# Kernel optimization log

Hardware: AMD Instinct MI355X
Metric: run time of the kernel (lower is better)

Reference implementation:

```python
import jax, jax.numpy as jnp
import numpy as np

DIM = 768
HEADS = 12
HD = DIM // HEADS
E = 8
R = 64
ALPHA = 128.0
LORA_SCALE = ALPHA / R  # 2.0
ENABLE_BITS = np.array([1.0, 0.0, 1.0], dtype=np.float32)  # LoRA on q and v slices of qkv


def setup_inputs() -> dict:
    key = jax.random.key(0)
    ks = jax.random.split(key, 8)
    x = jax.random.normal(ks[0], (2, 4096, DIM), jnp.float32)
    # base (frozen) weights, shared across experts; no biases (qkv_bias=False)
    Wqkv = jax.random.normal(ks[1], (3 * DIM, DIM), jnp.float32) * 0.02
    Wproj = jax.random.normal(ks[2], (DIM, DIM), jnp.float32) * 0.02
    # per-expert LoRA adapters. qkv: shared down-proj A, per-output-slice up-proj B,
    # masked by enable bits (q,k,v).
    Aqkv = jax.random.normal(ks[3], (E, R, DIM), jnp.float32) * 0.02
    Bqkv = jax.random.normal(ks[4], (E, 3, DIM, R), jnp.float32) * 0.02
    Bqkv = Bqkv * jnp.asarray(ENABLE_BITS)[None, :, None, None]
    Aproj = jax.random.normal(ks[5], (E, R, DIM), jnp.float32) * 0.02
    Bproj = jax.random.normal(ks[6], (E, DIM, R), jnp.float32) * 0.02
    expert_indices = np.arange(4, dtype=np.int64) % E  # static per-chunk routing
    chunk_sizes = np.array([1024, 1024, 1024, 1024], dtype=np.int64)
    return {"x": x, "Wqkv": Wqkv, "Aqkv": Aqkv, "Bqkv": Bqkv, "Wproj": Wproj,
            "Aproj": Aproj, "Bproj": Bproj, "expert_indices": expert_indices,
            "chunk_sizes": chunk_sizes}


def reference(x, Wqkv, Aqkv, Bqkv, Wproj, Aproj, Bproj, expert_indices, chunk_sizes):
    # chunk sizes / expert indices are static host-side routing metadata
    sizes = [int(c) for c in np.asarray(chunk_sizes)]
    eidx = [int(e) for e in np.asarray(expert_indices)]
    offs = np.concatenate([[0], np.cumsum(sizes)])
    B = x.shape[0]
    scale = HD ** -0.5
    last_k = None
    last_v = None
    outs = []
    for i, n in enumerate(sizes):
        xc = x[:, offs[i]:offs[i + 1]]            # [B, n, DIM]
        e = eidx[i]
        # LoRA-adapted qkv for this chunk's expert
        base = xc @ Wqkv.T                        # [B, n, 3*DIM]
        h = xc @ Aqkv[e].T                        # [B, n, R]
        delta = jnp.einsum('bnr,tdr->bntd', h, Bqkv[e]).reshape(B, n, 3 * DIM)
        qkv = (base + LORA_SCALE * delta).reshape(B, n, 3, HEADS, HD)
        qkv = qkv.transpose(2, 0, 3, 1, 4)        # [3, B, H, n, HD]
        q, k, v = qkv[0], qkv[1], qkv[2]
        if last_k is not None:                    # growing KV over chunks (chunk-causal)
            k = jnp.concatenate([last_k, k], axis=-2)
            v = jnp.concatenate([last_v, v], axis=-2)
        last_k, last_v = k, v
        attn = jax.nn.softmax(jnp.einsum('bhqd,bhkd->bhqk', q * scale, k), axis=-1)
        o = jnp.einsum('bhqk,bhkd->bhqd', attn, v)
        o = o.transpose(0, 2, 1, 3).reshape(B, n, DIM)
        # LoRA-adapted output projection for the same expert
        o = o @ Wproj.T + LORA_SCALE * ((o @ Aproj[e].T) @ Bproj[e].T)
        outs.append(o)
    return jnp.concatenate(outs, axis=1)          # [B, total, DIM]
```

## Files before the change

### kernel.cpp

```cpp
#include <hip/hip_runtime.h>
#include <hip/hip_bf16.h>
#include <math.h>

#define BATCH   2
#define SEQ     4096
#define DIMD    768
#define NHEADS  12
#define HDIM    64
#define RR      64
#define CHUNK   1024
#define NTOK    (BATCH * SEQ)
#define BHN     (BATCH * NHEADS)
#define KC2     2304
#define QSCALE  0.18033688011112042f

typedef __attribute__((ext_vector_type(8))) short short8;
typedef __attribute__((ext_vector_type(4))) float f32x4;

#define AS1 __attribute__((address_space(1)))
#define AS3 __attribute__((address_space(3)))

__device__ __forceinline__ void glds16(const void* g, void* l) {
    __builtin_amdgcn_global_load_lds((const AS1 unsigned int*)g,
                                     (AS3 unsigned int*)l, 16, 0, 0);
}

__device__ __forceinline__ unsigned pk2u(float a, float b) {
    float2 t; t.x = a; t.y = b;
    __hip_bfloat162 r = __float22bfloat162_rn(t);
    union { __hip_bfloat162 b2; unsigned u; } c; c.b2 = r;
    return c.u;
}
__device__ __forceinline__ float lo16f(unsigned p) { return __uint_as_float(p << 16); }
__device__ __forceinline__ float hi16f(unsigned p) { return __uint_as_float(p & 0xffff0000u); }

__global__ __launch_bounds__(256)
void combine_split(const float* __restrict__ W, const float* __restrict__ A,
                   const float* __restrict__ Bm, int NB,
                   unsigned short* __restrict__ out)
{
    const int tid = threadIdx.x;
    const int ty = tid >> 4, tx = tid & 15;
    const int f0 = blockIdx.x * 64, d0 = blockIdx.y * 64, e = blockIdx.z;

    __shared__ float Bb[64][68];
    __shared__ float Aa[64][68];

    const float* Ae = A + (long)e * RR * DIMD;
    const float* Be = Bm + (long)e * NB * RR;

    const int lrow = tid >> 2, lc = (tid & 3) * 16;
    #pragma unroll
    for (int u = 0; u < 16; u += 4) {
        *(float4*)&Bb[lrow][lc + u] = *(const float4*)&Be[(long)(f0 + lrow) * RR + lc + u];
        *(float4*)&Aa[lrow][lc + u] = *(const float4*)&Ae[(long)lrow * DIMD + d0 + lc + u];
    }
    __syncthreads();

    float acc[4][4] = {};
    #pragma unroll 4
    for (int r = 0; r < RR; r++) {
        const float4 bv = *(float4*)&Aa[r][tx * 4];
        #pragma unroll
        for (int i = 0; i < 4; i++) {
            const float av = Bb[ty + 16 * i][r];
            acc[i][0] = fmaf(av, bv.x, acc[i][0]);
            acc[i][1] = fmaf(av, bv.y, acc[i][1]);
            acc[i][2] = fmaf(av, bv.z, acc[i][2]);
            acc[i][3] = fmaf(av, bv.w, acc[i][3]);
        }
    }

    #pragma unroll
    for (int i = 0; i < 4; i++) {
        const int f = f0 + ty + 16 * i;
        const int d = d0 + tx * 4;
        unsigned short* o = out + ((long)e * NB + f) * KC2 + d;
        const float4 wv = *(const float4*)&W[(long)f * DIMD + d];
        const float v0 = wv.x + 2.0f * acc[i][0];
        const float v1 = wv.y + 2.0f * acc[i][1];
        const float v2 = wv.z + 2.0f * acc[i][2];
        const float v3 = wv.w + 2.0f * acc[i][3];
        uint2 hp, lp;
        hp.x = pk2u(v0, v1);
        hp.y = pk2u(v2, v3);
        lp.x = pk2u(v0 - lo16f(hp.x), v1 - hi16f(hp.x));
        lp.y = pk2u(v2 - lo16f(hp.y), v3 - hi16f(hp.y));
        *(uint2*)&o[0]    = hp;
        *(uint2*)&o[768]  = lp;
        *(uint2*)&o[1536] = hp;
    }
}

__global__ __launch_bounds__(192)
void build_xa2(const float* __restrict__ X, unsigned short* __restrict__ out)
{
    const int tok = blockIdx.x;
    const int j = threadIdx.x * 4;
    const float* xr = X + (long)tok * DIMD;
    unsigned short* o = out + (long)tok * KC2;
    float4 v = *(const float4*)&xr[j];
    uint2 hp, lp;
    hp.x = pk2u(v.x, v.y);
    hp.y = pk2u(v.z, v.w);
    lp.x = pk2u(v.x - lo16f(hp.x), v.y - hi16f(hp.x));
    lp.y = pk2u(v.z - lo16f(hp.y), v.w - hi16f(hp.y));
    *(uint2*)&o[j] = hp;
    *(uint2*)&o[768 + j] = hp;
    *(uint2*)&o[1536 + j] = lp;
}

template<bool SWAP>
__device__ __forceinline__ void gemm_core(const unsigned short* __restrict__ Ap,
                                          const unsigned short* __restrict__ Bp,
                                          unsigned short* lA, unsigned short* lB,
                                          f32x4 acc[4][4])
{
    const int tid = threadIdx.x;
    const int lane = tid & 63;
    const int wave = tid >> 6;
    const int n = lane & 15;
    const int quad = lane >> 4;
    const int wm = wave & 1, wn = wave >> 1;

    long soff[4];
    const int sldsoff = wave * 1024;
    #pragma unroll
    for (int iss = 0; iss < 4; iss++) {
        const int g = iss * 256 + tid;
        const int row = g >> 3;
        const int gc = (g & 7) ^ (row & 7);
        soff[iss] = (long)row * KC2 + gc * 8;
    }

    for (int k0 = 0; k0 < KC2; k0 += 64) {
        __syncthreads();
        #pragma unroll
        for (int iss = 0; iss < 4; iss++) {
            glds16(Ap + soff[iss] + k0, (char*)lA + iss * 4096 + sldsoff);
            glds16(Bp + soff[iss] + k0, (char*)lB + iss * 4096 + sldsoff);
        }
        __builtin_amdgcn_s_waitcnt(0);
        __syncthreads();

        #pragma unroll
        for (int kk = 0; kk < 2; kk++) {
            const int kg = kk * 4;
            short8 af[4], bfr[4];
            #pragma unroll
            for (int mt = 0; mt < 4; mt++) {
                const int r = wm * 64 + mt * 16 + n;
                const int p2 = (kg + quad) ^ (r & 7);
                af[mt] = *(const short8*)&lA[r * 64 + p2 * 8];
            }
            #pragma unroll
            for (int nt = 0; nt < 4; nt++) {
                const int r = wn * 64 + nt * 16 + n;
                const int p2 = (kg + quad) ^ (r & 7);
                bfr[nt] = *(const short8*)&lB[r * 64 + p2 * 8];
            }
            #pragma unroll
            for (int mt = 0; mt < 4; mt++)
                #pragma unroll
                for (int nt = 0; nt < 4; nt++) {
                    if (SWAP)
                        acc[mt][nt] = __builtin_amdgcn_mfma_f32_16x16x32_bf16(
                            bfr[nt], af[mt], acc[mt][nt], 0, 0, 0);
                    else
                        acc[mt][nt] = __builtin_amdgcn_mfma_f32_16x16x32_bf16(
                            af[mt], bfr[nt], acc[mt][nt], 0, 0, 0);
                }
        }
    }
}

__global__ __launch_bounds__(256)
void qkv_gemm(const unsigned short* __restrict__ A, const unsigned short* __restrict__ B,
              unsigned short* __restrict__ qpl, unsigned short* __restrict__ kpl,
              unsigned short* __restrict__ vpl)
{
    __shared__ __align__(16) unsigned short lA[128 * 64];
    __shared__ __align__(16) unsigned short lB[128 * 64];

    const int tid = threadIdx.x;
    const int lane = tid & 63;
    const int wave = tid >> 6;
    const int n = lane & 15;
    const int quad = lane >> 4;
    const int wm = wave & 1, wn = wave >> 1;
    const int id = blockIdx.x;

    f32x4 acc[4][4];
    #pragma unroll
    for (int i = 0; i < 4; i++)
        #pragma unroll
        for (int j = 0; j < 4; j++)
            acc[i][j] = (f32x4){0.f, 0.f, 0.f, 0.f};

    if (id < 768) {
        const int xcd = id & 7, loc = id >> 3;
        const int p = xcd * 6 + (loc >> 4), ml = loc & 15;
        const int e = p / 12, nb = p - e * 12;
        const int mb = ((ml >> 3) << 5) + e * 8 + (ml & 7);
        const int m0 = mb * 128, n0 = nb * 128;
        gemm_core<true>(A + (long)m0 * KC2, B + ((long)e * 2304 + n0) * KC2, lA, lB, acc);
        #pragma unroll
        for (int mt = 0; mt < 4; mt++) {
            #pragma unroll
            for (int nt = 0; nt < 4; nt++) {
                f32x4 a = acc[mt][nt];
                const int fb = n0 + wn * 64 + nt * 16 + quad * 4;
                const int t = fb >= 768 ? 1 : 0;
                const int rem = fb - t * 768;
                const int head = rem >> 6;
                const int d0 = rem & 63;
                const int token = m0 + wm * 64 + mt * 16 + n;
                const int b = token >> 12, s = token & (SEQ - 1);
                const int bh = b * NHEADS + head;
                const float sc = t ? 1.0f : QSCALE;
                unsigned short* dst = (t ? kpl : qpl) + ((long)(bh * SEQ + s)) * HDIM + d0;
                uint2 pk;
                pk.x = pk2u(a[0] * sc, a[1] * sc);
                pk.y = pk2u(a[2] * sc, a[3] * sc);
                *(uint2*)dst = pk;
            }
        }
    } else {
        const int id2 = id - 768;
        const int xcd = id2 & 7, loc = id2 >> 3;
        const int p = xcd * 3 + (loc >> 4), ml = loc & 15;
        const int e = p / 6, nb = p - e * 6;
        const int mb = ((ml >> 3) << 5) + e * 8 + (ml & 7);
        const int m0 = mb * 128, n0 = 1536 + nb * 128;
        gemm_core<false>(A + (long)m0 * KC2, B + ((long)e * 2304 + n0) * KC2, lA, lB, acc);
        #pragma unroll
        for (int mt = 0; mt < 4; mt++) {
            #pragma unroll
            for (int nt = 0; nt < 4; nt++) {
                f32x4 a = acc[mt][nt];
                const int f = n0 + wn * 64 + nt * 16 + n;
                const int head = (f - 1536) >> 6;
                const int d = f & 63;
                const int tok0 = m0 + wm * 64 + mt * 16 + quad * 4;
                const int b = tok0 >> 12, s0 = tok0 & (SEQ - 1);
                const int bh = b * NHEADS + head;
                unsigned short* dst = vpl + ((long)(bh * HDIM + d)) * SEQ + s0;
                uint2 pk;
                pk.x = pk2u(a[0], a[1]);
                pk.y = pk2u(a[2], a[3]);
                *(uint2*)dst = pk;
            }
        }
    }
}

__global__ __launch_bounds__(256)
void proj_gemm(const unsigned short* __restrict__ A, const unsigned short* __restrict__ B,
               float* __restrict__ outf)
{
    __shared__ __align__(16) unsigned short lA[128 * 64];
    __shared__ __align__(16) unsigned short lB[128 * 64];

    const int tid = threadIdx.x;
    const int lane = tid & 63;
    const int wave = tid >> 6;
    const int n = lane & 15;
    const int quad = lane >> 4;
    const int wm = wave & 1, wn = wave >> 1;

    const int id = blockIdx.x;
    const int xcd = id & 7, loc = id >> 3;
    const int p = xcd * 3 + (loc >> 4), ml = loc & 15;
    const int e = p / 6, nb = p - e * 6;
    const int mb = ((ml >> 3) << 5) + e * 8 + (ml & 7);
    const int m0 = mb * 128, n0 = nb * 128;

    f32x4 acc[4][4];
    #pragma unroll
    for (int i = 0; i < 4; i++)
        #pragma unroll
        for (int j = 0; j < 4; j++)
            acc[i][j] = (f32x4){0.f, 0.f, 0.f, 0.f};

    gemm_core<true>(A + (long)m0 * KC2, B + ((long)e * 768 + n0) * KC2, lA, lB, acc);

    #pragma unroll
    for (int mt = 0; mt < 4; mt++)
        #pragma unroll
        for (int nt = 0; nt < 4; nt++) {
            const int fb = n0 + wn * 64 + nt * 16 + quad * 4;
            const int token = m0 + wm * 64 + mt * 16 + n;
            *(f32x4*)&outf[(long)token * DIMD + fb] = acc[mt][nt];
        }
}

__global__ __launch_bounds__(512)
void attn_split(const unsigned short* __restrict__ qp,
                const unsigned short* __restrict__ kpl,
                const unsigned short* __restrict__ vtp,
                unsigned short* __restrict__ XA,
                float* __restrict__ pO, float* __restrict__ pl)
{
    __shared__ __align__(16) unsigned short lK[2 * 64 * 64];
    __shared__ __align__(16) unsigned short lV[2 * 64 * 64];
    __shared__ __align__(16) unsigned short lP[8][32 * 64];

    const int tid = threadIdx.x;
    const int lane = tid & 63;
    const int wave = tid >> 6;
    const int n = lane & 15;
    const int quad = lane >> 4;
    const int c7 = n & 7;

    const int id = blockIdx.x;
    const int xcd = id & 7;
    const int loc = id >> 3;
    const int sub = loc % 3;
    const int r2 = loc / 3;
    const int z = r2 % 6;
    const int qb = r2 / 6;
    const int bh = xcd * 3 + sub;

    int ci, ks0, klen, pidx;
    switch (z) {
        case 0:  ci = 3; ks0 = 0;    klen = 2048; pidx = 0;  break;
        case 1:  ci = 3; ks0 = 2048; klen = 2048; pidx = 1;  break;
        case 2:  ci = 2; ks0 = 0;    klen = 2048; pidx = 2;  break;
        case 3:  ci = 1; ks0 = 0;    klen = 2048; pidx = -1; break;
        case 4:  ci = 2; ks0 = 2048; klen = 1024; pidx = 3;  break;
        default: ci = 0; ks0 = 0;    klen = 1024; pidx = -1; break;
    }
    const int b = bh / NHEADS;
    const int h = bh - b * NHEADS;

    const long planeQK = (long)bh * SEQ * HDIM;
    const long planeVt = (long)bh * HDIM * SEQ;
    const int qch = qb * 256 + wave * 32;
    const int q0 = ci * CHUNK + qch;
    const int kend = ks0 + klen;

    long skoff, svoff;
    {
        const int row = tid >> 3;
        const int gc = (tid & 7) ^ (row & 7);
        skoff = (long)row * HDIM + gc * 8;
        svoff = (long)row * SEQ + gc * 8;
    }

    short8 qf[2][2];
    #pragma unroll
    for (int qt = 0; qt < 2; qt++)
        #pragma unroll
        for (int s = 0; s < 2; s++)
            qf[qt][s] = *(const short8*)&qp[planeQK + (long)(q0 + qt * 16 + n) * HDIM + s * 32 + quad * 8];

    const short8 ones8 = {0x3f80, 0x3f80, 0x3f80, 0x3f80, 0x3f80, 0x3f80, 0x3f80, 0x3f80};

    f32x4 acc[4][2];
    f32x4 accl[2];
    #pragma unroll
    for (int m2 = 0; m2 < 4; m2++) {
        acc[m2][0] = (f32x4){0.f, 0.f, 0.f, 0.f};
        acc[m2][1] = (f32x4){0.f, 0.f, 0.f, 0.f};
    }
    accl[0] = (f32x4){0.f, 0.f, 0.f, 0.f};
    accl[1] = (f32x4){0.f, 0.f, 0.f, 0.f};

    unsigned short* Pw = &lP[wave][0];

    glds16(kpl + planeQK + (long)ks0 * HDIM + skoff, (char*)lK + wave * 1024);
    glds16(vtp + planeVt + ks0 + svoff, (char*)lV + wave * 1024);
    __builtin_amdgcn_s_waitcnt(0);
    __syncthreads();

    int buf = 0;
    for (int k0 = ks0; k0 < kend; k0 += 64) {
        if (k0 + 64 < kend) {
            glds16(kpl + planeQK + (long)(k0 + 64) * HDIM + skoff,
                   (char*)lK + (buf ^ 1) * 8192 + wave * 1024);
            glds16(vtp + planeVt + (k0 + 64) + svoff,
                   (char*)lV + (buf ^ 1) * 8192 + wave * 1024);
        }
        const unsigned short* Kc = lK + buf * 4096;
        const unsigned short* Vc = lV + buf * 4096;

        f32x4 st[4][2];
        #pragma unroll
        for (int kt = 0; kt < 4; kt++) {
            st[kt][0] = (f32x4){0.f, 0.f, 0.f, 0.f};
            st[kt][1] = (f32x4){0.f, 0.f, 0.f, 0.f};
        }
        #pragma unroll
        for (int s = 0; s < 2; s++) {
            #pragma unroll
            for (int kt = 0; kt < 4; kt++) {
                const int gr = (s * 4 + quad) ^ c7;
                short8 kf = *(const short8*)&Kc[(kt * 16 + n) * 64 + gr * 8];
                st[kt][0] = __builtin_amdgcn_mfma_f32_16x16x32_bf16(kf, qf[0][s], st[kt][0], 0, 0, 0);
                st[kt][1] = __builtin_amdgcn_mfma_f32_16x16x32_bf16(kf, qf[1][s], st[kt][1], 0, 0, 0);
            }
        }

        #pragma unroll
        for (int qt = 0; qt < 2; qt++) {
            unsigned short* prow = Pw + (qt * 16 + n) * 64;
            #pragma unroll
            for (int kt = 0; kt < 4; kt++) {
                uint2 pkv;
                pkv.x = pk2u(__builtin_exp2f(st[kt][qt][0]), __builtin_exp2f(st[kt][qt][1]));
                pkv.y = pk2u(__builtin_exp2f(st[kt][qt][2]), __builtin_exp2f(st[kt][qt][3]));
                const int gsw = (2 * kt + (quad >> 1)) ^ c7;
                *(uint2*)&prow[gsw * 8 + (quad & 1) * 4] = pkv;
            }
        }

        #pragma unroll
        for (int hh = 0; hh < 2; hh++) {
            short8 pf[2];
            #pragma unroll
            for (int qt = 0; qt < 2; qt++) {
                const int gsw = (hh * 4 + quad) ^ c7;
                pf[qt] = *(const short8*)&Pw[(qt * 16 + n) * 64 + gsw * 8];
            }
            #pragma unroll
            for (int m2 = 0; m2 < 4; m2++) {
                const int gr = (hh * 4 + quad) ^ c7;
                short8 vf = *(const short8*)&Vc[(m2 * 16 + n) * 64 + gr * 8];
                acc[m2][0] = __builtin_amdgcn_mfma_f32_16x16x32_bf16(vf, pf[0], acc[m2][0], 0, 0, 0);
                acc[m2][1] = __builtin_amdgcn_mfma_f32_16x16x32_bf16(vf, pf[1], acc[m2][1], 0, 0, 0);
            }
            accl[0] = __builtin_amdgcn_mfma_f32_16x16x32_bf16(ones8, pf[0], accl[0], 0, 0, 0);
            accl[1] = __builtin_amdgcn_mfma_f32_16x16x32_bf16(ones8, pf[1], accl[1], 0, 0, 0);
        }

        __builtin_amdgcn_s_waitcnt(0);
        __syncthreads();
        buf ^= 1;
    }

    if (pidx < 0) {
        #pragma unroll
        for (int qt = 0; qt < 2; qt++) {
            const float inv = 1.0f / accl[qt][0];
            const int token = b * SEQ + q0 + qt * 16 + n;
            unsigned short* xrow = XA + (long)token * KC2;
            #pragma unroll
            for (int m2 = 0; m2 < 4; m2++) {
                const int d = h * HDIM + m2 * 16 + quad * 4;
                const float o0 = acc[m2][qt][0] * inv;
                const float o1 = acc[m2][qt][1] * inv;
                const float o2 = acc[m2][qt][2] * inv;
                const float o3 = acc[m2][qt][3] * inv;
                uint2 hp, lp;
                hp.x = pk2u(o0, o1);
                hp.y = pk2u(o2, o3);
                lp.x = pk2u(o0 - lo16f(hp.x), o1 - hi16f(hp.x));
                lp.y = pk2u(o2 - lo16f(hp.y), o3 - hi16f(hp.y));
                *(uint2*)&xrow[d] = hp;
                *(uint2*)&xrow[768 + d] = hp;
                *(uint2*)&xrow[1536 + d] = lp;
            }
        }
    } else {
        const long pq = (long)(pidx * BHN + bh) * 1024 + qch;
        #pragma unroll
        for (int qt = 0; qt < 2; qt++) {
            const long qoff = (pq + qt * 16 + n) * 64;
            #pragma unroll
            for (int m2 = 0; m2 < 4; m2++)
                *(f32x4*)&pO[qoff + m2 * 16 + quad * 4] = acc[m2][qt];
            if (quad == 0)
                pl[pq + qt * 16 + n] = accl[qt][0];
        }
    }
}

__global__ __launch_bounds__(256)
void attn_combine(const float* __restrict__ pO, const float* __restrict__ pl,
                  unsigned short* __restrict__ XA)
{
    const int t = threadIdx.x;
    const int g = blockIdx.x;
    const int ci = 2 + (g >> 3);
    const int qb = g & 7;
    const int bh = blockIdx.y;
    const int b = bh / NHEADS, h = bh - b * NHEADS;
    const int pA = (ci == 2) ? 2 : 0;
    const int pB = (ci == 2) ? 3 : 1;

    const int qrow = t >> 1;
    const int dh = (t & 1) * 32;
    const int qc = qb * 128 + qrow;
    const long iA = (long)(pA * BHN + bh) * 1024 + qc;
    const long iB = (long)(pB * BHN + bh) * 1024 + qc;
    const float inv = 1.0f / (pl[iA] + pl[iB]);
    const int token = b * SEQ + ci * CHUNK + qc;
    unsigned short* xrow = XA + (long)token * KC2 + h * HDIM + dh;

    #pragma unroll
    for (int u = 0; u < 8; u++) {
        const float4 a = *(const float4*)&pO[iA * 64 + dh + u * 4];
        const float4 c = *(const float4*)&pO[iB * 64 + dh + u * 4];
        const float o0 = (a.x + c.x) * inv;
        const float o1 = (a.y + c.y) * inv;
        const float o2 = (a.z + c.z) * inv;
        const float o3 = (a.w + c.w) * inv;
        uint2 hp, lp;
        hp.x = pk2u(o0, o1);
        hp.y = pk2u(o2, o3);
        lp.x = pk2u(o0 - lo16f(hp.x), o1 - hi16f(hp.x));
        lp.y = pk2u(o2 - lo16f(hp.y), o3 - hi16f(hp.y));
        *(uint2*)&xrow[u * 4] = hp;
        *(uint2*)&xrow[768 + u * 4] = hp;
        *(uint2*)&xrow[1536 + u * 4] = lp;
    }
}

extern "C" void kernel_launch(void* const* d_in, const int* in_sizes, int n_in,
                              void* d_out, int out_size, void* d_ws, size_t ws_size,
                              hipStream_t stream) {
    (void)in_sizes; (void)n_in; (void)out_size; (void)ws_size;
    const float* x     = (const float*)d_in[0];
    const float* Wqkv  = (const float*)d_in[1];
    const float* Aqkv  = (const float*)d_in[2];
    const float* Bqkv  = (const float*)d_in[3];
    const float* Wproj = (const float*)d_in[4];
    const float* Aproj = (const float*)d_in[5];
    const float* Bproj = (const float*)d_in[6];

    char* wsb = (char*)d_ws;
    unsigned short* XA   = (unsigned short*)(wsb);
    unsigned short* WBq  = (unsigned short*)(wsb + (38l << 20));
    float*          pO   = (float*)(wsb + (38l << 20));
    float*          pl   = (float*)(wsb + (63l << 20));
    unsigned short* WBp  = (unsigned short*)(wsb + (80l << 20));
    unsigned short* qpl  = (unsigned short*)(wsb + (94l << 20));
    unsigned short* kpl  = (unsigned short*)(wsb + (107l << 20));
    unsigned short* vpl  = (unsigned short*)(wsb + (120l << 20));

    dim3 blk(256);

    combine_split<<<dim3(36, 12, 4), blk, 0, stream>>>(Wqkv, Aqkv, Bqkv, 3 * DIMD, WBq);
    combine_split<<<dim3(12, 12, 4), blk, 0, stream>>>(Wproj, Aproj, Bproj, DIMD, WBp);
    build_xa2<<<dim3(NTOK), dim3(192), 0, stream>>>(x, XA);
    qkv_gemm<<<dim3(1152), blk, 0, stream>>>(XA, WBq, qpl, kpl, vpl);
    attn_split<<<dim3(576), dim3(512), 0, stream>>>(qpl, kpl, vpl, XA, pO, pl);
    attn_combine<<<dim3(16, BHN), blk, 0, stream>>>(pO, pl, XA);
    proj_gemm<<<dim3(384), blk, 0, stream>>>(XA, WBp, (float*)d_out);
}
```

Baseline: 426.9 us.

## Rebalance attention split into uniform 1024-key units with 64-query waves

The attention work split changes from uneven 1024/2048-key segments to uniform 1024-key segments (10 per head and query block, 960 blocks of 256 threads). Each wave now handles 64 queries, so every K/V tile in LDS is reused across more queries. The K/V double buffer is dropped in favour of single-buffered loads with a sync before each tile. The combine kernel now merges a variable number of partials and also covers chunk 1, and the two weight-combine launches are merged into one launch. Uniform work units should balance load across CUs, at the cost of exposed load latency, more partial-sum traffic and a workspace layout that was re-packed.

After: 510.6 us. +19.6%, slower.

```diff
diff --git a/kernel.cpp b/kernel.cpp
--- a/kernel.cpp
+++ b/kernel.cpp
@@ -35,13 +35,24 @@
 __device__ __forceinline__ float hi16f(unsigned p) { return __uint_as_float(p & 0xffff0000u); }
 
 __global__ __launch_bounds__(256)
-void combine_split(const float* __restrict__ W, const float* __restrict__ A,
-                   const float* __restrict__ Bm, int NB,
-                   unsigned short* __restrict__ out)
-{
+void combine_split(const float* __restrict__ Wq, const float* __restrict__ Aq,
+                   const float* __restrict__ Bq, unsigned short* __restrict__ outq,
+                   const float* __restrict__ Wp, const float* __restrict__ Ap,
+                   const float* __restrict__ Bp, unsigned short* __restrict__ outp)
+{
+    const int zz = blockIdx.z;
+    const int e = zz & 3;
+    const bool proj = zz >= 4;
+    const int NB = proj ? DIMD : 3 * DIMD;
+    if (proj && blockIdx.x >= 12) return;
+    const float* W = proj ? Wp : Wq;
+    const float* A = proj ? Ap : Aq;
+    const float* Bm = proj ? Bp : Bq;
+    unsigned short* out = proj ? outp : outq;
+
     const int tid = threadIdx.x;
     const int ty = tid >> 4, tx = tid & 15;
-    const int f0 = blockIdx.x * 64, d0 = blockIdx.y * 64, e = blockIdx.z;
+    const int f0 = blockIdx.x * 64, d0 = blockIdx.y * 64;
 
     __shared__ float Bb[64][68];
     __shared__ float Aa[64][68];
@@ -294,16 +305,16 @@
         }
 }
 
-__global__ __launch_bounds__(512)
+__global__ __launch_bounds__(256)
 void attn_split(const unsigned short* __restrict__ qp,
                 const unsigned short* __restrict__ kpl,
                 const unsigned short* __restrict__ vtp,
                 unsigned short* __restrict__ XA,
                 float* __restrict__ pO, float* __restrict__ pl)
 {
-    __shared__ __align__(16) unsigned short lK[2 * 64 * 64];
-    __shared__ __align__(16) unsigned short lV[2 * 64 * 64];
-    __shared__ __align__(16) unsigned short lP[8][32 * 64];
+    __shared__ __align__(16) unsigned short lK[64 * 64];
+    __shared__ __align__(16) unsigned short lV[64 * 64];
+    __shared__ __align__(16) unsigned short lP[4][64 * 64];
 
     const int tid = threadIdx.x;
     const int lane = tid & 63;
@@ -317,130 +328,122 @@
     const int loc = id >> 3;
     const int sub = loc % 3;
     const int r2 = loc / 3;
-    const int z = r2 % 6;
-    const int qb = r2 / 6;
+    const int z = r2 % 10;
+    const int qb = r2 / 10;
     const int bh = xcd * 3 + sub;
 
-    int ci, ks0, klen, pidx;
-    switch (z) {
-        case 0:  ci = 3; ks0 = 0;    klen = 2048; pidx = 0;  break;
-        case 1:  ci = 3; ks0 = 2048; klen = 2048; pidx = 1;  break;
-        case 2:  ci = 2; ks0 = 0;    klen = 2048; pidx = 2;  break;
-        case 3:  ci = 1; ks0 = 0;    klen = 2048; pidx = -1; break;
-        case 4:  ci = 2; ks0 = 2048; klen = 1024; pidx = 3;  break;
-        default: ci = 0; ks0 = 0;    klen = 1024; pidx = -1; break;
-    }
+    int ci, ks0, pidx;
+    if (z < 4)      { ci = 3; ks0 = z * 1024;       pidx = z; }
+    else if (z < 7) { ci = 2; ks0 = (z - 4) * 1024; pidx = z; }
+    else if (z < 9) { ci = 1; ks0 = (z - 7) * 1024; pidx = z; }
+    else            { ci = 0; ks0 = 0;              pidx = -1; }
     const int b = bh / NHEADS;
     const int h = bh - b * NHEADS;
 
     const long planeQK = (long)bh * SEQ * HDIM;
     const long planeVt = (long)bh * HDIM * SEQ;
-    const int qch = qb * 256 + wave * 32;
+    const int qch = qb * 256 + wave * 64;
     const int q0 = ci * CHUNK + qch;
-    const int kend = ks0 + klen;
-
-    long skoff, svoff;
-    {
-        const int row = tid >> 3;
-        const int gc = (tid & 7) ^ (row & 7);
-        skoff = (long)row * HDIM + gc * 8;
-        svoff = (long)row * SEQ + gc * 8;
-    }
-
-    short8 qf[2][2];
-    #pragma unroll
-    for (int qt = 0; qt < 2; qt++)
+
+    long skoff[2], svoff[2];
+    #pragma unroll
+    for (int p = 0; p < 2; p++) {
+        const int g = p * 256 + tid;
+        const int row = g >> 3;
+        const int gc = (g & 7) ^ (row & 7);
+        skoff[p] = (long)row * HDIM + gc * 8;
+        svoff[p] = (long)row * SEQ + gc * 8;
+    }
+
+    short8 qf[4][2];
+    #pragma unroll
+    for (int qt = 0; qt < 4; qt++)
         #pragma unroll
         for (int s = 0; s < 2; s++)
             qf[qt][s] = *(const short8*)&qp[planeQK + (long)(q0 + qt * 16 + n) * HDIM + s * 32 + quad * 8];
 
     const short8 ones8 = {0x3f80, 0x3f80, 0x3f80, 0x3f80, 0x3f80, 0x3f80, 0x3f80, 0x3f80};
 
-    f32x4 acc[4][2];
-    f32x4 accl[2];
-    #pragma unroll
-    for (int m2 = 0; m2 < 4; m2++) {
-        acc[m2][0] = (f32x4){0.f, 0.f, 0.f, 0.f};
-        acc[m2][1] = (f32x4){0.f, 0.f, 0.f, 0.f};
-    }
-    accl[0] = (f32x4){0.f, 0.f, 0.f, 0.f};
-    accl[1] = (f32x4){0.f, 0.f, 0.f, 0.f};
+    f32x4 acc[4][4];
+    f32x4 accl[4];
+    #pragma unroll
+    for (int m2 = 0; m2 < 4; m2++)
+        #pragma unroll
+        for (int qt = 0; qt < 4; qt++)
+            acc[m2][qt] = (f32x4){0.f, 0.f, 0.f, 0.f};
+    #pragma unroll
+    for (int qt = 0; qt < 4; qt++) accl[qt] = (f32x4){0.f, 0.f, 0.f, 0.f};
 
     unsigned short* Pw = &lP[wave][0];
 
-    glds16(kpl + planeQK + (long)ks0 * HDIM + skoff, (char*)lK + wave * 1024);
-    glds16(vtp + planeVt + ks0 + svoff, (char*)lV + wave * 1024);
-    __builtin_amdgcn_s_waitcnt(0);
-    __syncthreads();
-
-    int buf = 0;
-    for (int k0 = ks0; k0 < kend; k0 += 64) {
-        if (k0 + 64 < kend) {
-            glds16(kpl + planeQK + (long)(k0 + 64) * HDIM + skoff,
-                   (char*)lK + (buf ^ 1) * 8192 + wave * 1024);
-            glds16(vtp + planeVt + (k0 + 64) + svoff,
-                   (char*)lV + (buf ^ 1) * 8192 + wave * 1024);
-        }
-        const unsigned short* Kc = lK + buf * 4096;
-        const unsigned short* Vc = lV + buf * 4096;
-
-        f32x4 st[4][2];
-        #pragma unroll
-        for (int kt = 0; kt < 4; kt++) {
-            st[kt][0] = (f32x4){0.f, 0.f, 0.f, 0.f};
-            st[kt][1] = (f32x4){0.f, 0.f, 0.f, 0.f};
-        }
-        #pragma unroll
-        for (int s = 0; s < 2; s++) {
+    for (int kt0 = 0; kt0 < 16; kt0++) {
+        const int k0 = ks0 + kt0 * 64;
+        __syncthreads();
+        glds16(kpl + planeQK + (long)k0 * HDIM + skoff[0], (char*)lK + wave * 1024);
+        glds16(kpl + planeQK + (long)k0 * HDIM + skoff[1], (char*)lK + 4096 + wave * 1024);
+        glds16(vtp + planeVt + k0 + svoff[0], (char*)lV + wave * 1024);
+        glds16(vtp + planeVt + k0 + svoff[1], (char*)lV + 4096 + wave * 1024);
+        __builtin_amdgcn_s_waitcnt(0);
+        __syncthreads();
+
+        #pragma unroll
+        for (int half = 0; half < 2; half++) {
+            f32x4 st[4][2];
             #pragma unroll
             for (int kt = 0; kt < 4; kt++) {
-                const int gr = (s * 4 + quad) ^ c7;
-                short8 kf = *(const short8*)&Kc[(kt * 16 + n) * 64 + gr * 8];
-                st[kt][0] = __builtin_amdgcn_mfma_f32_16x16x32_bf16(kf, qf[0][s], st[kt][0], 0, 0, 0);
-                st[kt][1] = __builtin_amdgcn_mfma_f32_16x16x32_bf16(kf, qf[1][s], st[kt][1], 0, 0, 0);
-            }
-        }
-
-        #pragma unroll
-        for (int qt = 0; qt < 2; qt++) {
-            unsigned short* prow = Pw + (qt * 16 + n) * 64;
-            #pragma unroll
-            for (int kt = 0; kt < 4; kt++) {
-                uint2 pkv;
-                pkv.x = pk2u(__builtin_exp2f(st[kt][qt][0]), __builtin_exp2f(st[kt][qt][1]));
-                pkv.y = pk2u(__builtin_exp2f(st[kt][qt][2]), __builtin_exp2f(st[kt][qt][3]));
-                const int gsw = (2 * kt + (quad >> 1)) ^ c7;
-                *(uint2*)&prow[gsw * 8 + (quad & 1) * 4] = pkv;
+                st[kt][0] = (f32x4){0.f, 0.f, 0.f, 0.f};
+                st[kt][1] = (f32x4){0.f, 0.f, 0.f, 0.f};
+            }
+            #pragma unroll
+            for (int s = 0; s < 2; s++) {
+                #pragma unroll
+                for (int kt = 0; kt < 4; kt++) {
+                    const int gr = (s * 4 + quad) ^ c7;
+                    short8 kf = *(const short8*)&lK[(kt * 16 + n) * 64 + gr * 8];
+                    st[kt][0] = __builtin_amdgcn_mfma_f32_16x16x32_bf16(kf, qf[2 * half][s],     st[kt][0], 0, 0, 0);
+                    st[kt][1] = __builtin_amdgcn_mfma_f32_16x16x32_bf16(kf, qf[2 * half + 1][s], st[kt][1], 0, 0, 0);
+                }
+            }
+            #pragma unroll
+            for (int q2 = 0; q2 < 2; q2++) {
+                const int qt = 2 * half + q2;
+                unsigned short* prow = Pw + (qt * 16 + n) * 64;
+                #pragma unroll
+                for (int kt = 0; kt < 4; kt++) {
+                    uint2 pkv;
+                    pkv.x = pk2u(__builtin_exp2f(st[kt][q2][0]), __builtin_exp2f(st[kt][q2][1]));
+                    pkv.y = pk2u(__builtin_exp2f(st[kt][q2][2]), __builtin_exp2f(st[kt][q2][3]));
+                    const int gsw = (2 * kt + (quad >> 1)) ^ c7;
+                    *(uint2*)&prow[gsw * 8 + (quad & 1) * 4] = pkv;
+                }
             }
         }
 
         #pragma unroll
         for (int hh = 0; hh < 2; hh++) {
-            short8 pf[2];
-            #pragma unroll
-            for (int qt = 0; qt < 2; qt++) {
+            short8 pf[4];
+            #pragma unroll
+            for (int qt = 0; qt < 4; qt++) {
                 const int gsw = (hh * 4 + quad) ^ c7;
                 pf[qt] = *(const short8*)&Pw[(qt * 16 + n) * 64 + gsw * 8];
             }
             #pragma unroll
             for (int m2 = 0; m2 < 4; m2++) {
                 const int gr = (hh * 4 + quad) ^ c7;
-                short8 vf = *(const short8*)&Vc[(m2 * 16 + n) * 64 + gr * 8];
-                acc[m2][0] = __builtin_amdgcn_mfma_f32_16x16x32_bf16(vf, pf[0], acc[m2][0], 0, 0, 0);
-                acc[m2][1] = __builtin_amdgcn_mfma_f32_16x16x32_bf16(vf, pf[1], acc[m2][1], 0, 0, 0);
-            }
-            accl[0] = __builtin_amdgcn_mfma_f32_16x16x32_bf16(ones8, pf[0], accl[0], 0, 0, 0);
-            accl[1] = __builtin_amdgcn_mfma_f32_16x16x32_bf16(ones8, pf[1], accl[1], 0, 0, 0);
-        }
-
-        __builtin_amdgcn_s_waitcnt(0);
-        __syncthreads();
-        buf ^= 1;
+                short8 vf = *(const short8*)&lV[(m2 * 16 + n) * 64 + gr * 8];
+                #pragma unroll
+                for (int qt = 0; qt < 4; qt++)
+                    acc[m2][qt] = __builtin_amdgcn_mfma_f32_16x16x32_bf16(vf, pf[qt], acc[m2][qt], 0, 0, 0);
+            }
+            #pragma unroll
+            for (int qt = 0; qt < 4; qt++)
+                accl[qt] = __builtin_amdgcn_mfma_f32_16x16x32_bf16(ones8, pf[qt], accl[qt], 0, 0, 0);
+        }
     }
 
     if (pidx < 0) {
         #pragma unroll
-        for (int qt = 0; qt < 2; qt++) {
+        for (int qt = 0; qt < 4; qt++) {
             const float inv = 1.0f / accl[qt][0];
             const int token = b * SEQ + q0 + qt * 16 + n;
             unsigned short* xrow = XA + (long)token * KC2;
@@ -464,7 +467,7 @@
     } else {
         const long pq = (long)(pidx * BHN + bh) * 1024 + qch;
         #pragma unroll
-        for (int qt = 0; qt < 2; qt++) {
+        for (int qt = 0; qt < 4; qt++) {
             const long qoff = (pq + qt * 16 + n) * 64;
             #pragma unroll
             for (int m2 = 0; m2 < 4; m2++)
@@ -481,30 +484,33 @@
 {
     const int t = threadIdx.x;
     const int g = blockIdx.x;
-    const int ci = 2 + (g >> 3);
+    const int ci = 1 + (g >> 3);
     const int qb = g & 7;
     const int bh = blockIdx.y;
     const int b = bh / NHEADS, h = bh - b * NHEADS;
-    const int pA = (ci == 2) ? 2 : 0;
-    const int pB = (ci == 2) ? 3 : 1;
+    const int pbase = (ci == 3) ? 0 : (ci == 2) ? 4 : 7;
+    const int cnt = ci + 1;
 
     const int qrow = t >> 1;
     const int dh = (t & 1) * 32;
     const int qc = qb * 128 + qrow;
-    const long iA = (long)(pA * BHN + bh) * 1024 + qc;
-    const long iB = (long)(pB * BHN + bh) * 1024 + qc;
-    const float inv = 1.0f / (pl[iA] + pl[iB]);
+
+    float lsum = 0.f;
+    for (int i = 0; i < cnt; i++)
+        lsum += pl[(long)((pbase + i) * BHN + bh) * 1024 + qc];
+    const float inv = 1.0f / lsum;
     const int token = b * SEQ + ci * CHUNK + qc;
     unsigned short* xrow = XA + (long)token * KC2 + h * HDIM + dh;
 
     #pragma unroll
     for (int u = 0; u < 8; u++) {
-        const float4 a = *(const float4*)&pO[iA * 64 + dh + u * 4];
-        const float4 c = *(const float4*)&pO[iB * 64 + dh + u * 4];
-        const float o0 = (a.x + c.x) * inv;
-        const float o1 = (a.y + c.y) * inv;
-        const float o2 = (a.z + c.z) * inv;
-        const float o3 = (a.w + c.w) * inv;
+        float o0 = 0.f, o1 = 0.f, o2 = 0.f, o3 = 0.f;
+        for (int i = 0; i < cnt; i++) {
+            const long base = ((long)((pbase + i) * BHN + bh) * 1024 + qc) * 64 + dh + u * 4;
+            const float4 a = *(const float4*)&pO[base];
+            o0 += a.x; o1 += a.y; o2 += a.z; o3 += a.w;
+        }
+        o0 *= inv; o1 *= inv; o2 *= inv; o3 *= inv;
         uint2 hp, lp;
         hp.x = pk2u(o0, o1);
         hp.y = pk2u(o2, o3);
@@ -530,21 +536,21 @@
 
     char* wsb = (char*)d_ws;
     unsigned short* XA   = (unsigned short*)(wsb);
-    unsigned short* WBq  = (unsigned short*)(wsb + (38l << 20));
-    float*          pO   = (float*)(wsb + (38l << 20));
-    float*          pl   = (float*)(wsb + (63l << 20));
-    unsigned short* WBp  = (unsigned short*)(wsb + (80l << 20));
-    unsigned short* qpl  = (unsigned short*)(wsb + (94l << 20));
-    unsigned short* kpl  = (unsigned short*)(wsb + (107l << 20));
-    unsigned short* vpl  = (unsigned short*)(wsb + (120l << 20));
+    float*          pl   = (float*)(wsb + (36l << 20));
+    unsigned short* qpl  = (unsigned short*)(wsb + (37l << 20));
+    unsigned short* kpl  = (unsigned short*)(wsb + (50l << 20));
+    unsigned short* vpl  = (unsigned short*)(wsb + (63l << 20));
+    unsigned short* WBp  = (unsigned short*)(wsb + (76l << 20));
+    unsigned short* WBq  = (unsigned short*)(wsb + (90l << 20));
+    float*          pO   = (float*)(wsb + (90l << 20));
 
     dim3 blk(256);
 
-    combine_split<<<dim3(36, 12, 4), blk, 0, stream>>>(Wqkv, Aqkv, Bqkv, 3 * DIMD, WBq);
-    combine_split<<<dim3(12, 12, 4), blk, 0, stream>>>(Wproj, Aproj, Bproj, DIMD, WBp);
+    combine_split<<<dim3(36, 12, 8), blk, 0, stream>>>(
+        Wqkv, Aqkv, Bqkv, WBq, Wproj, Aproj, Bproj, WBp);
     build_xa2<<<dim3(NTOK), dim3(192), 0, stream>>>(x, XA);
     qkv_gemm<<<dim3(1152), blk, 0, stream>>>(XA, WBq, qpl, kpl, vpl);
-    attn_split<<<dim3(576), dim3(512), 0, stream>>>(qpl, kpl, vpl, XA, pO, pl);
-    attn_combine<<<dim3(16, BHN), blk, 0, stream>>>(pO, pl, XA);
+    attn_split<<<dim3(960), blk, 0, stream>>>(qpl, kpl, vpl, XA, pO, pl);
+    attn_combine<<<dim3(24, BHN), blk, 0, stream>>>(pO, pl, XA);
     proj_gemm<<<dim3(384), blk, 0, stream>>>(XA, WBp, (float*)d_out);
 }
```
